# Kernel tuning notes

Measured on AMD Instinct MI355X. Metric: run time of the kernel, lower is better.

Reference implementation:

```python
import jax, jax.numpy as jnp
import numpy as np

D_MODEL = 1024
N_HEADS = 16
DIM_HEAD = D_MODEL // N_HEADS
SCALE = DIM_HEAD ** -0.5


def setup_inputs() -> dict:
    key = jax.random.key(0)
    ks = jax.random.split(key, 7)
    B, N = 2, 2048
    q = jax.random.normal(ks[0], (B, N, D_MODEL), dtype=jnp.float32)
    # boolean mask: True = masked out; keep sparse so softmax rows stay valid
    mask = jax.random.bernoulli(ks[1], 0.1, (B, N, N))
    s = D_MODEL ** -0.5
    Wq = jax.random.normal(ks[2], (D_MODEL, D_MODEL), dtype=jnp.float32) * s
    Wk = jax.random.normal(ks[3], (D_MODEL, D_MODEL), dtype=jnp.float32) * s
    Wv = jax.random.normal(ks[4], (D_MODEL, D_MODEL), dtype=jnp.float32) * s
    Wo = jax.random.normal(ks[5], (D_MODEL, D_MODEL), dtype=jnp.float32) * s
    bo = jnp.zeros((D_MODEL,), dtype=jnp.float32)
    return {"q": q, "mask": mask, "Wq": Wq, "Wk": Wk, "Wv": Wv, "Wo": Wo, "bo": bo}


def reference(q, mask, Wq, Wk, Wv, Wo, bo):
    B, N, D = q.shape
    # self-attention: memory = q. nn.Linear applies x @ W.T (W is [out, in]).
    qh = (q @ Wq.T) * SCALE
    kh = q @ Wk.T
    vh = q @ Wv.T
    # b n (h d) -> b h n d
    qh = qh.reshape(B, N, N_HEADS, DIM_HEAD).transpose(0, 2, 1, 3)
    kh = kh.reshape(B, N, N_HEADS, DIM_HEAD).transpose(0, 2, 1, 3)
    vh = vh.reshape(B, N, N_HEADS, DIM_HEAD).transpose(0, 2, 1, 3)
    scores = jnp.einsum('bhid,bhjd->bhij', qh, kh)  # [B,H,N,N]
    mask_value = -jnp.finfo(scores.dtype).max
    scores = jnp.where(mask[:, None, :, :], mask_value, scores)
    attn = jax.nn.softmax(scores, axis=-1)
    o = jnp.einsum('bhij,bhjd->bhid', attn, vh)
    o = o.transpose(0, 2, 1, 3).reshape(B, N, D)  # b h n d -> b n (h d)
    return o @ Wo.T + bo
```

## Files before the change

### kernel.cpp

```cpp
#include <hip/hip_runtime.h>
#include <hip/hip_bf16.h>

typedef float fx4 __attribute__((ext_vector_type(4)));
typedef short s16x8 __attribute__((ext_vector_type(8)));

#define NSEQ 2048
#define DM   1024
#define NH   16
#define DH   64
#define MROWS 4096
#define NWORDS (2 * NSEQ * (NSEQ / 64))

#define QK_SCALE (0.125f * 1.44269504088896f)

__device__ __forceinline__ unsigned short f2bf(float f) {
    union { float f; unsigned u; } c; c.f = f;
    unsigned u = c.u;
    unsigned r = u + 0x7FFFu + ((u >> 16) & 1u);
    return (unsigned short)(r >> 16);
}

__device__ __forceinline__ float exp2_fast(float x) {
#if __has_builtin(__builtin_amdgcn_exp2f)
    return __builtin_amdgcn_exp2f(x);
#else
    return exp2f(x);
#endif
}

__device__ __forceinline__ fx4 zero4() {
    fx4 z; z[0] = 0.f; z[1] = 0.f; z[2] = 0.f; z[3] = 0.f; return z;
}

__device__ __forceinline__ void gload16(const void* g, void* l) {
    __builtin_amdgcn_global_load_lds(
        (const __attribute__((address_space(1))) unsigned int*)g,
        (__attribute__((address_space(3))) unsigned int*)l,
        16, 0, 0);
}

__global__ void cvt_kernel(const float* __restrict__ in,
                           unsigned short* __restrict__ out, int n4) {
    int i = blockIdx.x * blockDim.x + threadIdx.x;
    if (i >= n4) return;
    float4 v = reinterpret_cast<const float4*>(in)[i];
    ushort4 o;
    o.x = f2bf(v.x); o.y = f2bf(v.y); o.z = f2bf(v.z); o.w = f2bf(v.w);
    reinterpret_cast<ushort4*>(out)[i] = o;
}

__global__ void cvt4_kernel(const float* __restrict__ w0, const float* __restrict__ w1,
                            const float* __restrict__ w2, const float* __restrict__ w3,
                            unsigned short* __restrict__ o0, unsigned short* __restrict__ o1,
                            unsigned short* __restrict__ o2, unsigned short* __restrict__ o3) {
    const float* in; unsigned short* out;
    switch (blockIdx.y) {
        case 0:  in = w0; out = o0; break;
        case 1:  in = w1; out = o1; break;
        case 2:  in = w2; out = o2; break;
        default: in = w3; out = o3; break;
    }
    int i = blockIdx.x * blockDim.x + threadIdx.x;
    float4 v = reinterpret_cast<const float4*>(in)[i];
    ushort4 o;
    o.x = f2bf(v.x); o.y = f2bf(v.y); o.z = f2bf(v.z); o.w = f2bf(v.w);
    reinterpret_cast<ushort4*>(out)[i] = o;
}

__global__ void mask_detect(const unsigned int* __restrict__ m, int* __restrict__ flag) {
    unsigned mx = 0;
    int stride = gridDim.x * blockDim.x;
    for (int i = blockIdx.x * blockDim.x + threadIdx.x; i < (2 * NSEQ * NSEQ) / 4; i += stride) {
        unsigned v = m[i];
        mx = v > mx ? v : mx;
    }
    if (__any(mx > 1u)) {
        if ((threadIdx.x & 63) == 0) atomicOr(flag, 1);
    }
}

__global__ void mask_pack(const void* __restrict__ mask, const int* __restrict__ mflag,
                          unsigned long long* __restrict__ packed) {
    const int flg  = mflag[0];
    const int lane = threadIdx.x & 63;
    const int wpb  = blockDim.x >> 6;
    const int perm = (lane & 3) * 16 + (lane >> 2);
    size_t w = (size_t)blockIdx.x * wpb + (threadIdx.x >> 6);
    const size_t stride = (size_t)gridDim.x * wpb;
    for (; w < NWORDS; w += stride) {
        size_t elem = (w >> 5) * (size_t)NSEQ + (size_t)(w & 31) * 64 + perm;
        int mv = flg ? (int)((const unsigned char*)mask)[elem]
                     : ((const int*)mask)[elem];
        unsigned long long bits = __ballot(mv != 0);
        if (lane == 0) packed[w] = bits;
    }
}

__global__ __launch_bounds__(256) void gemm_qkv(
        const unsigned short* __restrict__ A,
        const unsigned short* __restrict__ Wq,
        const unsigned short* __restrict__ Wk,
        const unsigned short* __restrict__ Wv,
        unsigned short* __restrict__ Qh,
        unsigned short* __restrict__ Kh,
        unsigned short* __restrict__ VhT) {
    __shared__ unsigned short As[128 * 32];
    __shared__ unsigned short Bs[128 * 32];

    const int tid  = threadIdx.x;
    const int lane = tid & 63;
    const int w    = tid >> 6;
    const int lr   = lane & 15;
    const int lg   = lane >> 4;
    const int wr   = (w >> 1) * 64;
    const int wc   = (w & 1) * 64;
    const int rowbase = blockIdx.y * 128;
    const int seg     = blockIdx.x >> 3;
    const int cb      = (blockIdx.x & 7) * 128;
    const unsigned short* W = seg == 0 ? Wq : (seg == 1 ? Wk : Wv);
    const float scale = seg == 0 ? QK_SCALE : 1.0f;

    fx4 acc[4][4];
#pragma unroll
    for (int i = 0; i < 4; i++)
#pragma unroll
        for (int j = 0; j < 4; j++) acc[i][j] = zero4();

    for (int k0 = 0; k0 < DM; k0 += 32) {
        __syncthreads();
#pragma unroll
        for (int i = 0; i < 2; i++) {
            int j = i * 256 + w * 64 + lane;
            int r = j >> 2, c8 = (j & 3) * 8;
            gload16(A + (size_t)(rowbase + r) * DM + k0 + c8,
                    As + (size_t)(i * 256 + w * 64) * 8);
            gload16(W + (size_t)(cb + r) * DM + k0 + c8,
                    Bs + (size_t)(i * 256 + w * 64) * 8);
        }
        __syncthreads();

        s16x8 af[4], bf[4];
#pragma unroll
        for (int mi = 0; mi < 4; mi++)
            af[mi] = *reinterpret_cast<const s16x8*>(&As[(wr + mi * 16 + lr) * 32 + 8 * lg]);
#pragma unroll
        for (int ni = 0; ni < 4; ni++)
            bf[ni] = *reinterpret_cast<const s16x8*>(&Bs[(wc + ni * 16 + lr) * 32 + 8 * lg]);
#pragma unroll
        for (int mi = 0; mi < 4; mi++)
#pragma unroll
            for (int ni = 0; ni < 4; ni++)
                acc[mi][ni] = __builtin_amdgcn_mfma_f32_16x16x32_bf16(af[mi], bf[ni], acc[mi][ni], 0, 0, 0);
    }

#pragma unroll
    for (int mi = 0; mi < 4; mi++) {
#pragma unroll
        for (int ni = 0; ni < 4; ni++) {
#pragma unroll
            for (int v = 0; v < 4; v++) {
                int m    = rowbase + wr + mi * 16 + lg * 4 + v;
                int cseg = cb + wc + ni * 16 + lr;
                float val = acc[mi][ni][v] * scale;
                int b = m >> 11, nseq = m & 2047;
                int h = cseg >> 6, dh = cseg & 63;
                if (seg < 2) {
                    unsigned short* dst = seg == 0 ? Qh : Kh;
                    dst[((size_t)(b * NH + h) * NSEQ + nseq) * DH + dh] = f2bf(val);
                } else {
                    VhT[((size_t)(b * NH + h) * DH + dh) * NSEQ + nseq] = f2bf(val);
                }
            }
        }
    }
}

__global__ __launch_bounds__(256) void gemm_out(
        const unsigned short* __restrict__ A,
        const unsigned short* __restrict__ W,
        float* __restrict__ out,
        const float* __restrict__ bias) {
    __shared__ unsigned short As[128 * 32];
    __shared__ unsigned short Bs[128 * 32];

    const int tid  = threadIdx.x;
    const int lane = tid & 63;
    const int w    = tid >> 6;
    const int lr   = lane & 15;
    const int lg   = lane >> 4;
    const int wr   = (w >> 1) * 64;
    const int wc   = (w & 1) * 64;
    const int rowbase = blockIdx.y * 128;
    const int colbase = blockIdx.x * 128;

    fx4 acc[4][4];
#pragma unroll
    for (int i = 0; i < 4; i++)
#pragma unroll
        for (int j = 0; j < 4; j++) acc[i][j] = zero4();

    for (int k0 = 0; k0 < DM; k0 += 32) {
        __syncthreads();
#pragma unroll
        for (int i = 0; i < 2; i++) {
            int j = i * 256 + w * 64 + lane;
            int r = j >> 2, c8 = (j & 3) * 8;
            gload16(A + (size_t)(rowbase + r) * DM + k0 + c8,
                    As + (size_t)(i * 256 + w * 64) * 8);
            gload16(W + (size_t)(colbase + r) * DM + k0 + c8,
                    Bs + (size_t)(i * 256 + w * 64) * 8);
        }
        __syncthreads();

        s16x8 af[4], bf[4];
#pragma unroll
        for (int mi = 0; mi < 4; mi++)
            af[mi] = *reinterpret_cast<const s16x8*>(&As[(wr + mi * 16 + lr) * 32 + 8 * lg]);
#pragma unroll
        for (int ni = 0; ni < 4; ni++)
            bf[ni] = *reinterpret_cast<const s16x8*>(&Bs[(wc + ni * 16 + lr) * 32 + 8 * lg]);
#pragma unroll
        for (int mi = 0; mi < 4; mi++)
#pragma unroll
            for (int ni = 0; ni < 4; ni++)
                acc[mi][ni] = __builtin_amdgcn_mfma_f32_16x16x32_bf16(af[mi], bf[ni], acc[mi][ni], 0, 0, 0);
    }

#pragma unroll
    for (int mi = 0; mi < 4; mi++)
#pragma unroll
        for (int ni = 0; ni < 4; ni++)
#pragma unroll
            for (int v = 0; v < 4; v++) {
                int m = rowbase + wr + mi * 16 + lg * 4 + v;
                int c = colbase + wc + ni * 16 + lr;
                out[(size_t)m * DM + c] = acc[mi][ni][v] + bias[c];
            }
}

__global__ __launch_bounds__(256) void attn_kernel(
        const unsigned short* __restrict__ Qh,
        const unsigned short* __restrict__ Kh,
        const unsigned short* __restrict__ VhT,
        const unsigned long long* __restrict__ Mp,
        unsigned short* __restrict__ Obuf) {
    __shared__ unsigned short Ks[64 * 64];
    __shared__ unsigned short Vs[64 * 64];
    __shared__ unsigned short Ps[4][16][72];

    const int tid  = threadIdx.x;
    const int lane = tid & 63;
    const int w    = tid >> 6;
    const int lr   = lane & 15;
    const int lg   = lane >> 4;
    const int qbase = blockIdx.x * 64;
    const int bh    = blockIdx.y;
    const int b     = bh >> 4;
    const int h     = bh & 15;

    s16x8 qf[2];
    const size_t qrow0 = (size_t)bh * NSEQ + qbase + w * 16 + lr;
#pragma unroll
    for (int kk = 0; kk < 2; kk++)
        qf[kk] = *reinterpret_cast<const s16x8*>(Qh + qrow0 * DH + kk * 32 + 8 * lg);

    float mrow[4], lrow[4];
    fx4 acc[4];
#pragma unroll
    for (int v = 0; v < 4; v++) { mrow[v] = -3.0e38f; lrow[v] = 0.f; }
#pragma unroll
    for (int t = 0; t < 4; t++) acc[t] = zero4();

    const int qglob = qbase + w * 16 + lg * 4;
    const size_t mrow0 = ((size_t)b * NSEQ + qglob) * (NSEQ / 64);

    for (int kv0 = 0; kv0 < NSEQ; kv0 += 64) {
        __syncthreads();
#pragma unroll
        for (int i = 0; i < 2; i++) {
            int u  = tid + i * 256;
            int r  = u >> 3, cu = u & 7;
            int cs = cu ^ (r & 7);
            s16x8 kv = *reinterpret_cast<const s16x8*>(Kh + ((size_t)bh * NSEQ + kv0 + r) * DH + cu * 8);
            *reinterpret_cast<s16x8*>(&Ks[r * 64 + cs * 8]) = kv;
            s16x8 vv = *reinterpret_cast<const s16x8*>(VhT + ((size_t)bh * DH + r) * NSEQ + kv0 + cu * 8);
            *reinterpret_cast<s16x8*>(&Vs[r * 64 + cs * 8]) = vv;
        }

        unsigned mbits[4];
#pragma unroll
        for (int v = 0; v < 4; v++) {
            unsigned long long pw = Mp[mrow0 + (size_t)v * (NSEQ / 64) + (kv0 >> 6)];
            mbits[v] = (unsigned)(pw >> (lr * 4)) & 15u;
        }
        __syncthreads();

        fx4 s[4];
#pragma unroll
        for (int t = 0; t < 4; t++) {
            s[t] = zero4();
#pragma unroll
            for (int kk = 0; kk < 2; kk++) {
                int r  = t * 16 + lr;
                int cu = kk * 4 + lg;
                int cs = cu ^ (r & 7);
                s16x8 kf = *reinterpret_cast<const s16x8*>(&Ks[r * 64 + cs * 8]);
                s[t] = __builtin_amdgcn_mfma_f32_16x16x32_bf16(qf[kk], kf, s[t], 0, 0, 0);
            }
        }

        float tmax[4];
#pragma unroll
        for (int v = 0; v < 4; v++) tmax[v] = -3.0e38f;
#pragma unroll
        for (int t = 0; t < 4; t++)
#pragma unroll
            for (int v = 0; v < 4; v++) {
                float sv = ((mbits[v] >> t) & 1u) ? -3.0e38f : s[t][v];
                s[t][v] = sv;
                tmax[v] = fmaxf(tmax[v], sv);
            }
#pragma unroll
        for (int off = 1; off < 16; off <<= 1)
#pragma unroll
            for (int v = 0; v < 4; v++)
                tmax[v] = fmaxf(tmax[v], __shfl_xor(tmax[v], off));

        float sc[4], psum[4];
#pragma unroll
        for (int v = 0; v < 4; v++) {
            float mn = fmaxf(mrow[v], tmax[v]);
            sc[v]    = exp2_fast(mrow[v] - mn);
            mrow[v]  = mn;
            psum[v]  = 0.f;
        }
#pragma unroll
        for (int t = 0; t < 4; t++)
#pragma unroll
            for (int v = 0; v < 4; v++) {
                float p = exp2_fast(s[t][v] - mrow[v]);
                s[t][v] = p;
                psum[v] += p;
            }
#pragma unroll
        for (int off = 1; off < 16; off <<= 1)
#pragma unroll
            for (int v = 0; v < 4; v++)
                psum[v] += __shfl_xor(psum[v], off);
#pragma unroll
        for (int v = 0; v < 4; v++) lrow[v] = lrow[v] * sc[v] + psum[v];
#pragma unroll
        for (int t = 0; t < 4; t++)
#pragma unroll
            for (int v = 0; v < 4; v++) acc[t][v] *= sc[v];

#pragma unroll
        for (int t = 0; t < 4; t++)
#pragma unroll
            for (int v = 0; v < 4; v++)
                Ps[w][lg * 4 + v][t * 16 + lr] = f2bf(s[t][v]);

#pragma unroll
        for (int kk = 0; kk < 2; kk++) {
            s16x8 pf = *reinterpret_cast<const s16x8*>(&Ps[w][lr][kk * 32 + 8 * lg]);
#pragma unroll
            for (int t = 0; t < 4; t++) {
                int r  = t * 16 + lr;
                int cu = kk * 4 + lg;
                int cs = cu ^ (r & 7);
                s16x8 vf = *reinterpret_cast<const s16x8*>(&Vs[r * 64 + cs * 8]);
                acc[t] = __builtin_amdgcn_mfma_f32_16x16x32_bf16(pf, vf, acc[t], 0, 0, 0);
            }
        }
    }

#pragma unroll
    for (int t = 0; t < 4; t++)
#pragma unroll
        for (int v = 0; v < 4; v++) {
            int q = qglob + v;
            int d = t * 16 + lr;
            Obuf[((size_t)b * NSEQ + q) * DM + h * DH + d] = f2bf(acc[t][v] / lrow[v]);
        }
}

extern "C" void kernel_launch(void* const* d_in, const int* in_sizes, int n_in,
                              void* d_out, int out_size, void* d_ws, size_t ws_size,
                              hipStream_t stream) {
    const float* q    = (const float*)d_in[0];
    const void*  mask = (const void*)d_in[1];
    const float* Wq   = (const float*)d_in[2];
    const float* Wk   = (const float*)d_in[3];
    const float* Wv   = (const float*)d_in[4];
    const float* Wo   = (const float*)d_in[5];
    const float* bo   = (const float*)d_in[6];
    float* out = (float*)d_out;

    char* ws = (char*)d_ws;
    const size_t MB = 1024 * 1024;
    unsigned short* qbf  = (unsigned short*)(ws + 0);
    unsigned long long* packed = (unsigned long long*)(ws + 0);
    unsigned short* Wqb  = (unsigned short*)(ws + 8  * MB);
    unsigned short* Wkb  = (unsigned short*)(ws + 10 * MB);
    unsigned short* Wvb  = (unsigned short*)(ws + 12 * MB);
    unsigned short* Wob  = (unsigned short*)(ws + 14 * MB);
    unsigned short* Qh   = (unsigned short*)(ws + 16 * MB);
    unsigned short* Kh   = (unsigned short*)(ws + 24 * MB);
    unsigned short* VhT  = (unsigned short*)(ws + 32 * MB);
    unsigned short* Obuf = (unsigned short*)(ws + 40 * MB);
    int*            flag = (int*)(ws + 56 * MB);

    hipMemsetAsync(flag, 0, 4, stream);
    mask_detect<<<1024, 256, 0, stream>>>((const unsigned int*)mask, flag);

    cvt_kernel<<<4096, 256, 0, stream>>>(q, qbf, (2 * NSEQ * DM) / 4);
    cvt4_kernel<<<dim3(1024, 4), 256, 0, stream>>>(Wq, Wk, Wv, Wo, Wqb, Wkb, Wvb, Wob);

    gemm_qkv<<<dim3(24, 32), 256, 0, stream>>>(qbf, Wqb, Wkb, Wvb, Qh, Kh, VhT);

    mask_pack<<<1024, 256, 0, stream>>>(mask, flag, packed);

    attn_kernel<<<dim3(NSEQ / 64, 32), 256, 0, stream>>>(Qh, Kh, VhT, packed, Obuf);

    gemm_out<<<dim3(8, 32), 256, 0, stream>>>(Obuf, Wob, out, bo);
}
```

Before: 306.5 us.

## Double-buffer attention K/V via async LDS loads and transpose score layout

The attention kernel now double-buffers K and V tiles in shared memory, loading the next tile with global_load_lds while computing on the current one, with a single barrier per iteration. Scores are computed transposed (K as the A operand), so each lane owns a single query row, and row max/sum need only two cross-lane shuffles. Rescaling of the accumulator is skipped unless the max grows by more than a threshold (lazy rescale), and P is packed to bf16 with a hardware convert instruction into a swizzled LDS layout. Workgroups are remapped across the grid, and the mask bit permutation is changed to match the new layout. The lazy rescale adds some numerical risk, and the doubled LDS footprint may lower occupancy.

Result: faster. 258.5 us (-15.7%).

```diff
diff --git a/kernel.cpp b/kernel.cpp
--- a/kernel.cpp
+++ b/kernel.cpp
@@ -26,6 +26,12 @@
 #else
     return exp2f(x);
 #endif
+}
+
+__device__ __forceinline__ unsigned cvt_pk_bf16(float a, float b) {
+    unsigned r;
+    asm("v_cvt_pk_bf16_f32 %0, %1, %2" : "=v"(r) : "v"(a), "v"(b));
+    return r;
 }
 
 __device__ __forceinline__ fx4 zero4() {
@@ -84,7 +90,7 @@
     const int flg  = mflag[0];
     const int lane = threadIdx.x & 63;
     const int wpb  = blockDim.x >> 6;
-    const int perm = (lane & 3) * 16 + (lane >> 2);
+    const int perm = ((lane >> 2) & 3) * 16 + ((lane >> 4) & 3) * 4 + (lane & 3);
     size_t w = (size_t)blockIdx.x * wpb + (threadIdx.x >> 6);
     const size_t stride = (size_t)gridDim.x * wpb;
     for (; w < NWORDS; w += stride) {
@@ -244,56 +250,57 @@
         const unsigned short* __restrict__ VhT,
         const unsigned long long* __restrict__ Mp,
         unsigned short* __restrict__ Obuf) {
-    __shared__ unsigned short Ks[64 * 64];
-    __shared__ unsigned short Vs[64 * 64];
-    __shared__ unsigned short Ps[4][16][72];
+    __shared__ unsigned short Ks[2][64 * 64];
+    __shared__ unsigned short Vs[2][64 * 64];
+    __shared__ __align__(16) unsigned int Ps[4][16 * 32];
 
     const int tid  = threadIdx.x;
     const int lane = tid & 63;
     const int w    = tid >> 6;
     const int lr   = lane & 15;
     const int lg   = lane >> 4;
-    const int qbase = blockIdx.x * 64;
-    const int bh    = blockIdx.y;
+
+    const int wg    = ((blockIdx.x & 7) << 7) + (blockIdx.x >> 3);
+    const int qbase = (wg & 31) << 6;
+    const int bh    = wg >> 5;
     const int b     = bh >> 4;
     const int h     = bh & 15;
 
     s16x8 qf[2];
-    const size_t qrow0 = (size_t)bh * NSEQ + qbase + w * 16 + lr;
+    const size_t qrow = (size_t)bh * NSEQ + qbase + w * 16 + lr;
 #pragma unroll
     for (int kk = 0; kk < 2; kk++)
-        qf[kk] = *reinterpret_cast<const s16x8*>(Qh + qrow0 * DH + kk * 32 + 8 * lg);
-
-    float mrow[4], lrow[4];
+        qf[kk] = *reinterpret_cast<const s16x8*>(Qh + qrow * DH + kk * 32 + 8 * lg);
+
+    float mreg = -3.0e38f, lrow = 0.f;
     fx4 acc[4];
 #pragma unroll
-    for (int v = 0; v < 4; v++) { mrow[v] = -3.0e38f; lrow[v] = 0.f; }
-#pragma unroll
     for (int t = 0; t < 4; t++) acc[t] = zero4();
 
-    const int qglob = qbase + w * 16 + lg * 4;
-    const size_t mrow0 = ((size_t)b * NSEQ + qglob) * (NSEQ / 64);
-
-    for (int kv0 = 0; kv0 < NSEQ; kv0 += 64) {
-        __syncthreads();
+    const size_t mbase = ((size_t)b * NSEQ + qbase + w * 16 + lr) * (NSEQ / 64);
+
+    auto stage = [&](int d, int kv0) {
 #pragma unroll
         for (int i = 0; i < 2; i++) {
-            int u  = tid + i * 256;
-            int r  = u >> 3, cu = u & 7;
-            int cs = cu ^ (r & 7);
-            s16x8 kv = *reinterpret_cast<const s16x8*>(Kh + ((size_t)bh * NSEQ + kv0 + r) * DH + cu * 8);
-            *reinterpret_cast<s16x8*>(&Ks[r * 64 + cs * 8]) = kv;
-            s16x8 vv = *reinterpret_cast<const s16x8*>(VhT + ((size_t)bh * DH + r) * NSEQ + kv0 + cu * 8);
-            *reinterpret_cast<s16x8*>(&Vs[r * 64 + cs * 8]) = vv;
-        }
-
-        unsigned mbits[4];
-#pragma unroll
-        for (int v = 0; v < 4; v++) {
-            unsigned long long pw = Mp[mrow0 + (size_t)v * (NSEQ / 64) + (kv0 >> 6)];
-            mbits[v] = (unsigned)(pw >> (lr * 4)) & 15u;
-        }
-        __syncthreads();
+            int u  = i * 256 + w * 64 + lane;
+            int r  = u >> 3, cs = u & 7;
+            int cu = cs ^ (r & 7);
+            gload16(Kh + ((size_t)bh * NSEQ + kv0 + r) * DH + cu * 8,
+                    &Ks[d][(size_t)(i * 256 + w * 64) * 8]);
+            gload16(VhT + ((size_t)bh * DH + r) * NSEQ + kv0 + cu * 8,
+                    &Vs[d][(size_t)(i * 256 + w * 64) * 8]);
+        }
+    };
+
+    stage(0, 0);
+    __syncthreads();
+
+    for (int it = 0; it < NSEQ / 64; it++) {
+        const int cur = it & 1;
+        if (it < NSEQ / 64 - 1) stage(cur ^ 1, (it + 1) << 6);
+
+        unsigned long long pwm = Mp[mbase + it];
+        unsigned mb = (unsigned)((pwm >> (lg * 16)) & 0xFFFFull);
 
         fx4 s[4];
 #pragma unroll
@@ -302,86 +309,88 @@
 #pragma unroll
             for (int kk = 0; kk < 2; kk++) {
                 int r  = t * 16 + lr;
-                int cu = kk * 4 + lg;
-                int cs = cu ^ (r & 7);
-                s16x8 kf = *reinterpret_cast<const s16x8*>(&Ks[r * 64 + cs * 8]);
-                s[t] = __builtin_amdgcn_mfma_f32_16x16x32_bf16(qf[kk], kf, s[t], 0, 0, 0);
-            }
-        }
-
-        float tmax[4];
-#pragma unroll
-        for (int v = 0; v < 4; v++) tmax[v] = -3.0e38f;
+                int cs = (kk * 4 + lg) ^ (r & 7);
+                s16x8 kf = *reinterpret_cast<const s16x8*>(&Ks[cur][r * 64 + cs * 8]);
+                s[t] = __builtin_amdgcn_mfma_f32_16x16x32_bf16(kf, qf[kk], s[t], 0, 0, 0);
+            }
+        }
+
+        float tmax = -3.0e38f;
 #pragma unroll
         for (int t = 0; t < 4; t++)
 #pragma unroll
             for (int v = 0; v < 4; v++) {
-                float sv = ((mbits[v] >> t) & 1u) ? -3.0e38f : s[t][v];
+                float sv = (mb & (1u << (t * 4 + v))) ? -3.0e38f : s[t][v];
                 s[t][v] = sv;
-                tmax[v] = fmaxf(tmax[v], sv);
-            }
-#pragma unroll
-        for (int off = 1; off < 16; off <<= 1)
-#pragma unroll
-            for (int v = 0; v < 4; v++)
-                tmax[v] = fmaxf(tmax[v], __shfl_xor(tmax[v], off));
-
-        float sc[4], psum[4];
-#pragma unroll
-        for (int v = 0; v < 4; v++) {
-            float mn = fmaxf(mrow[v], tmax[v]);
-            sc[v]    = exp2_fast(mrow[v] - mn);
-            mrow[v]  = mn;
-            psum[v]  = 0.f;
-        }
+                tmax = fmaxf(tmax, sv);
+            }
+        tmax = fmaxf(tmax, __shfl_xor(tmax, 16));
+        tmax = fmaxf(tmax, __shfl_xor(tmax, 32));
+
+        if (__any(tmax > mreg + 8.0f)) {
+            float mn = fmaxf(mreg, tmax);
+            float sc = exp2_fast(mreg - mn);
+            mreg = mn;
+            lrow *= sc;
+#pragma unroll
+            for (int v = 0; v < 4; v++) {
+                float scv = __shfl(sc, (lane & 48) | (lg * 4 + v));
+#pragma unroll
+                for (int t = 0; t < 4; t++) acc[t][v] *= scv;
+            }
+        }
+
+        float psum = 0.f;
 #pragma unroll
         for (int t = 0; t < 4; t++)
 #pragma unroll
             for (int v = 0; v < 4; v++) {
-                float p = exp2_fast(s[t][v] - mrow[v]);
+                float p = exp2_fast(s[t][v] - mreg);
                 s[t][v] = p;
-                psum[v] += p;
-            }
-#pragma unroll
-        for (int off = 1; off < 16; off <<= 1)
-#pragma unroll
-            for (int v = 0; v < 4; v++)
-                psum[v] += __shfl_xor(psum[v], off);
-#pragma unroll
-        for (int v = 0; v < 4; v++) lrow[v] = lrow[v] * sc[v] + psum[v];
-#pragma unroll
-        for (int t = 0; t < 4; t++)
-#pragma unroll
-            for (int v = 0; v < 4; v++) acc[t][v] *= sc[v];
-
-#pragma unroll
-        for (int t = 0; t < 4; t++)
-#pragma unroll
-            for (int v = 0; v < 4; v++)
-                Ps[w][lg * 4 + v][t * 16 + lr] = f2bf(s[t][v]);
+                psum += p;
+            }
+        psum += __shfl_xor(psum, 16);
+        psum += __shfl_xor(psum, 32);
+        lrow += psum;
+
+#pragma unroll
+        for (int t = 0; t < 4; t++) {
+            unsigned p0 = cvt_pk_bf16(s[t][0], s[t][1]);
+            unsigned p1 = cvt_pk_bf16(s[t][2], s[t][3]);
+            int idx = (t * 8 + lg * 2) ^ ((lr & 7) << 2);
+            *reinterpret_cast<unsigned long long*>(&Ps[w][lr * 32 + idx]) =
+                ((unsigned long long)p1 << 32) | p0;
+        }
 
 #pragma unroll
         for (int kk = 0; kk < 2; kk++) {
-            s16x8 pf = *reinterpret_cast<const s16x8*>(&Ps[w][lr][kk * 32 + 8 * lg]);
+            int ridx = (kk * 16 + lg * 4) ^ ((lr & 7) << 2);
+            union { uint4 u; s16x8 v; } cvt;
+            cvt.u = *reinterpret_cast<const uint4*>(&Ps[w][lr * 32 + ridx]);
+            s16x8 pf = cvt.v;
 #pragma unroll
             for (int t = 0; t < 4; t++) {
                 int r  = t * 16 + lr;
-                int cu = kk * 4 + lg;
-                int cs = cu ^ (r & 7);
-                s16x8 vf = *reinterpret_cast<const s16x8*>(&Vs[r * 64 + cs * 8]);
+                int cs = (kk * 4 + lg) ^ (r & 7);
+                s16x8 vf = *reinterpret_cast<const s16x8*>(&Vs[cur][r * 64 + cs * 8]);
                 acc[t] = __builtin_amdgcn_mfma_f32_16x16x32_bf16(pf, vf, acc[t], 0, 0, 0);
             }
         }
-    }
-
-#pragma unroll
-    for (int t = 0; t < 4; t++)
-#pragma unroll
-        for (int v = 0; v < 4; v++) {
-            int q = qglob + v;
+
+        __syncthreads();
+    }
+
+#pragma unroll
+    for (int v = 0; v < 4; v++) {
+        float lq  = __shfl(lrow, (lane & 48) | (lg * 4 + v));
+        float inv = 1.0f / lq;
+        int q = qbase + w * 16 + lg * 4 + v;
+#pragma unroll
+        for (int t = 0; t < 4; t++) {
             int d = t * 16 + lr;
-            Obuf[((size_t)b * NSEQ + q) * DM + h * DH + d] = f2bf(acc[t][v] / lrow[v]);
-        }
+            Obuf[((size_t)b * NSEQ + q) * DM + h * DH + d] = f2bf(acc[t][v] * inv);
+        }
+    }
 }
 
 extern "C" void kernel_launch(void* const* d_in, const int* in_sizes, int n_in,
@@ -420,7 +429,7 @@
 
     mask_pack<<<1024, 256, 0, stream>>>(mask, flag, packed);
 
-    attn_kernel<<<dim3(NSEQ / 64, 32), 256, 0, stream>>>(Qh, Kh, VhT, packed, Obuf);
+    attn_kernel<<<1024, 256, 0, stream>>>(Qh, Kh, VhT, packed, Obuf);
 
     gemm_out<<<dim3(8, 32), 256, 0, stream>>>(Obuf, Wob, out, bo);
 }
```
